# Optimization experiments

Hardware: AMD Instinct MI355X
Metric: run time of the kernel (lower is better)

## Reference

```python
import jax, jax.numpy as jnp
import numpy as np
import math

D = 768
H = 12
HD = D // H  # 64


def setup_inputs() -> dict:
    key = jax.random.key(0)
    ks = jax.random.split(key, 8)
    B, S = 32, 127
    desc = jax.random.normal(ks[0], (B, S, D), dtype=jnp.float32)
    nv = jax.random.normal(ks[1], (B, S + 1, D), dtype=jnp.float32)
    def xavier(k, shape):
        fan_in, fan_out = shape[1], shape[0]
        gain = 1.0 / math.sqrt(2.0)
        limit = gain * math.sqrt(6.0 / (fan_in + fan_out))
        return jax.random.uniform(k, shape, jnp.float32, -limit, limit)
    Wq = xavier(ks[2], (D, D)); bq = jnp.zeros((D,), jnp.float32)
    Wk = xavier(ks[3], (D, D)); bk = jnp.zeros((D,), jnp.float32)
    Wv = xavier(ks[4], (D, D)); bv = jnp.zeros((D,), jnp.float32)
    # attn_proj: Linear(3*head_dim, 1)
    Wa = xavier(ks[5], (1, 3 * HD))[0]  # [3*HD]
    ba = jnp.zeros((), jnp.float32)
    return {
        "desc_embeddings": desc,
        "name_value_embeddings": nv,
        "Wq": Wq, "bq": bq, "Wk": Wk, "bk": bk, "Wv": Wv, "bv": bv,
        "Wa": Wa, "ba": ba,
    }


def _forward(desc_embeddings, name_value_embeddings, Wq, bq, Wk, bk, Wv, bv, Wa, ba):
    B, new_seq, _ = name_value_embeddings.shape
    S = new_seq - 1

    # adjacency: var-var all ones, CLS->Var row = 1, Var->CLS col = 0, CLS->CLS = 0
    adj = jnp.zeros((new_seq, new_seq), jnp.float32)
    adj = adj.at[1:, 1:].set(1.0)
    adj = adj.at[0, 1:].set(1.0)
    adj = jnp.broadcast_to(adj, (B, new_seq, new_seq))

    # q,k,v: [B, H, new_seq, HD]
    def proj(W, b):
        y = name_value_embeddings @ W.T + b
        return y.reshape(B, new_seq, H, HD).transpose(0, 2, 1, 3)
    q = proj(Wq, bq); k = proj(Wk, bk); v = proj(Wv, bv)

    # attn_proj weight split: [q_part | k_part | edge_part], each [HD]
    wq_a, wk_a, we_a = Wa[:HD], Wa[HD:2 * HD], Wa[2 * HD:]

    # q/k scalar contributions per (b,h,i) and (b,h,j)
    lq = jnp.einsum('bhid,d->bhi', q, wq_a)  # [B,H,new_seq]
    lk = jnp.einsum('bhjd,d->bhj', k, wk_a)  # [B,H,new_seq]

    # edge_attr[b,i,j] per head h (head slice of concat[node_i_desc, node_j_desc]):
    # edge vector = concat(desc_i, desc_j)[h*HD:(h+1)*HD] viewed as [H, HD] of 2D dims.
    # concat(desc_i, desc_j) has 2D dims -> reshaped to [H, HD] means head h takes
    # slice [h*HD:(h+1)*HD] of the 2D-dim concat. Heads 0..H/2-1 come from desc_i,
    # heads H/2..H-1 come from desc_j. Compute edge dot with we_a accordingly.
    # desc_full[b,t] : [B,S,D]. Build per-head contributions:
    # for h < H//2: edge slice = desc_i[h*HD:(h+1)*HD]  -> depends only on i
    # for h >= H//2: edge slice = desc_j[(h-H//2)*HD:(h-H//2+1)*HD] -> depends only on j
    desc_heads = desc_embeddings.reshape(B, S, H // 2, 2 * HD)  # wrong split; do directly
    # Direct: per head h, slice indices into the 2D concat vector
    dh = desc_embeddings.reshape(B, S, H, HD)  # desc split into H chunks of HD (covers D = H*HD)
    # concat(desc_i,desc_j) reshaped to [H,HD]: heads 0..H/2-1 use dh_i[:, :, h],
    # heads H/2..H-1 use dh_j[:, :, h - H/2]
    e_dot = jnp.einsum('bshd,d->bsh', dh, jnp.broadcast_to(we_a, (HD,)))  # placeholder, recompute per head below
    # per-head edge scalar contribution for var-var edges:
    ei = jnp.einsum('bshd,d->bhs', dh, we_a)  # contribution if head slice comes from desc at position s
    Hh = H // 2
    # var-var logits edge part: for h<Hh depends on i; for h>=Hh depends on j
    le_i = ei[:, :Hh, :]   # [B,Hh,S] depends on i (row)
    le_j = ei[:, Hh:, :]   # [B,Hh,S] depends on j (col)

    # CLS edges: cls_edge_attr = concat(desc, desc) at position t (the var index)
    # row 0 (CLS->var j): edge = concat(desc_j, desc_j) -> head h slice:
    #   h<Hh: dh_j[h]; h>=Hh: dh_j[h-Hh]  -> scalar ei[b,h,j] with h mapped
    e_cls = jnp.concatenate([ei[:, :Hh, :], ei[:, :Hh, :]], axis=1) * 0  # init
    e_cls = jnp.concatenate([le_i, le_i], axis=1)  # [B,H,S]: head h<Hh uses dh[h], h>=Hh uses dh[h-Hh]
    # note ei[:, :Hh] corresponds to dh chunks 0..Hh-1 ; for h>=Hh slice is dh[h-Hh] -> same le_i

    # Assemble full logits [B,H,new_seq,new_seq]
    logits = lq[:, :, :, None] + lk[:, :, None, :]
    # edge contributions (only where adj==1; edge_attr zeroed elsewhere by mask mult)
    edge = jnp.zeros((B, H, new_seq, new_seq), jnp.float32)
    # var-var block [1:,1:]
    ev = jnp.zeros((B, H, S, S), jnp.float32)
    ev = ev + jnp.pad(le_i, ((0, 0), (0, Hh), (0, 0)))[:, :, :, None] * 0  # keep shapes
    ev_i = jnp.concatenate([le_i, jnp.zeros_like(le_j)], axis=1)  # h<Hh: i-dependent
    ev_j = jnp.concatenate([jnp.zeros_like(le_i), le_j], axis=1)  # h>=Hh: j-dependent
    ev = ev_i[:, :, :, None] + ev_j[:, :, None, :]  # [B,H,S,S]
    edge = edge.at[:, :, 1:, 1:].set(ev)
    # CLS row (0, 1:): cls_edge = concat(desc_j,desc_j); j = column var
    edge = edge.at[:, :, 0, 1:].set(e_cls)
    # CLS col (1:, 0): cls_edge = concat(desc_i,desc_i) BUT adj[:,1:,0]=0 so edge_attr
    # multiplied by adj -> zero; also masked out. edge stays 0, but torch zeroes it too.
    # mask edge by adjacency (edge_attr *= adj)
    edge = edge * adj[:, None, :, :]
    logits = logits + edge + ba

    mask = (adj[:, None, :, :] == 0).astype(jnp.float32) * -1e9
    logits = logits + mask
    attn = jax.nn.softmax(logits, axis=-1)  # [B,H,new_seq,new_seq]
    ctx = jnp.einsum('bhij,bhjd->bhid', attn, v)
    basis_outputs = ctx.transpose(0, 2, 1, 3)  # [B,new_seq,H,HD]
    return basis_outputs, attn


def reference(desc_embeddings, name_value_embeddings, Wq, bq, Wk, bk, Wv, bv, Wa, ba):
    return _forward(desc_embeddings, name_value_embeddings, Wq, bq, Wk, bk, Wv, bv, Wa, ba)
```

## Files before the change

### kernel.cpp

```cpp
#include <hip/hip_runtime.h>

#define NB 32
#define NS 128
#define SD 127
#define ND 768
#define NH 12
#define HD 64

__device__ inline float wredSum(float v){
  #pragma unroll
  for (int off=32; off>0; off>>=1) v += __shfl_xor(v, off);
  return v;
}
__device__ inline float wredMax(float v){
  #pragma unroll
  for (int off=32; off>0; off>>=1) v = fmaxf(v, __shfl_xor(v, off));
  return v;
}

__global__ __launch_bounds__(256)
void fold_ei(const float* __restrict__ Wk, const float* __restrict__ bk,
             const float* __restrict__ desc, const float* __restrict__ Wa,
             float* __restrict__ uk, float* __restrict__ bkdot,
             float* __restrict__ ei){
  int blk = blockIdx.x, t = threadIdx.x;
  int wave = t >> 6, lane = t & 63;
  if (blk < 144){
    __shared__ float red[4][64];
    int h = blk/12, cb = blk%12;
    int c0 = t & 63, dg = t >> 6;
    const float* base = Wk + (size_t)(h*HD + dg*16)*ND + cb*64 + c0;
    float acc = 0.f;
    #pragma unroll
    for (int i=0;i<16;++i) acc += base[(size_t)i*ND] * Wa[64 + dg*16 + i];
    red[dg][c0] = acc;
    __syncthreads();
    if (dg==0) uk[h*ND + cb*64 + c0] = red[0][c0]+red[1][c0]+red[2][c0]+red[3][c0];
    if (blk==0 && t < NH){
      float a = 0.f;
      for (int d=0; d<64; ++d) a += bk[t*HD+d]*Wa[64+d];
      bkdot[t] = a;
    }
  } else {
    int bs = blk - 144;
    int b = bs / SD, s = bs % SD;
    float wea = Wa[128 + lane];
    const float* row = desc + (size_t)bs * ND;
    #pragma unroll
    for (int hh=0; hh<3; ++hh){
      int h = wave + hh*4;
      float v = row[h*HD + lane] * wea;
      v = wredSum(v);
      if (lane==0) ei[(size_t)(b*NH + h)*NS + s] = v;
    }
  }
}

__global__ __launch_bounds__(256)
void lk_kernel(const float* __restrict__ nv, const float* __restrict__ uk,
               const float* __restrict__ bkdot, float* __restrict__ lk){
  __shared__ __align__(16) float S[4*ND];
  int blk = blockIdx.x, t = threadIdx.x, wave = t>>6, lane = t&63;
  float ukr[3][12], bkd[3];
  #pragma unroll
  for (int hh=0; hh<3; ++hh){
    int h = wave*3 + hh;
    bkd[hh] = bkdot[h];
    #pragma unroll
    for (int k=0;k<12;++k) ukr[hh][k] = uk[h*ND + lane + 64*k];
  }
  int j0 = blk*4;
  const float4* src = (const float4*)(nv + (size_t)j0*ND);
  ((float4*)S)[t]     = src[t];
  ((float4*)S)[t+256] = src[t+256];
  ((float4*)S)[t+512] = src[t+512];
  __syncthreads();
  float acc[12];
  #pragma unroll
  for (int rr=0; rr<4; ++rr)
    #pragma unroll
    for (int hh=0; hh<3; ++hh){
      float a = 0.f;
      #pragma unroll
      for (int k=0;k<12;++k) a += S[rr*ND + lane + 64*k]*ukr[hh][k];
      acc[rr*3+hh] = a;
    }
  #pragma unroll
  for (int i=0;i<12;++i) acc[i] = wredSum(acc[i]);
  if (lane == 0){
    int b = j0 >> 7, jb = j0 & 127;
    #pragma unroll
    for (int rr=0; rr<4; ++rr)
      #pragma unroll
      for (int hh=0; hh<3; ++hh)
        lk[(size_t)(b*NH + wave*3 + hh)*NS + jb + rr] = acc[rr*3+hh] + bkd[hh];
  }
}

__global__ __launch_bounds__(256)
void msoft_attn(const float* __restrict__ nv, const float* __restrict__ lk,
                const float* __restrict__ ei, float* __restrict__ m_part,
                float* __restrict__ out){
  int blk = blockIdx.x;
  int b = blk >> 4, jg = blk & 15;
  int t = threadIdx.x, wave = t >> 6, lane = t & 63;
  __shared__ float slk[NH*NS];
  __shared__ float sei[NH*NS];
  __shared__ float wf[24][NS];
  for (int i=t; i<NH*NS; i+=256) slk[i] = lk[(size_t)b*NH*NS + i];
  for (int i=t; i<NH*NS; i+=256) sei[i] = ei[(size_t)b*NH*NS + i];
  __syncthreads();
  #pragma unroll
  for (int rr=0; rr<6; ++rr){
    int r = wave*6 + rr;
    int h = r >> 1, which = r & 1;
    const float* eirow = (which==0) ? (sei + (h%6)*NS) : (sei + h*NS);
    float g = (which==0) ? 1.f : (h>=6 ? 1.f : 0.f);
    float x0 = (lane>=1) ? slk[h*NS+lane] + g*eirow[lane-1] : -3.0e38f;
    float x1 = slk[h*NS+lane+64] + g*eirow[lane+63];
    float mm = wredMax(fmaxf(x0,x1));
    float e0 = (lane>=1) ? __expf(x0-mm) : 0.f;
    float e1 = __expf(x1-mm);
    float s  = wredSum(e0+e1);
    float inv = 1.f/s;
    wf[r][lane]    = e0*inv;
    wf[r][lane+64] = e1*inv;
  }
  __syncthreads();
  if (t < 192){
    const float4* nvb = (const float4*)(nv + ((size_t)b*NS + jg*8)*ND);
    float4 acc[24];
    #pragma unroll
    for (int r=0;r<24;++r) acc[r] = make_float4(0.f,0.f,0.f,0.f);
    #pragma unroll
    for (int jj=0; jj<8; ++jj){
      float4 x = nvb[jj*192 + t];
      int j = jg*8 + jj;
      #pragma unroll
      for (int r=0;r<24;++r){
        float wr = wf[r][j];
        acc[r].x += wr*x.x; acc[r].y += wr*x.y;
        acc[r].z += wr*x.z; acc[r].w += wr*x.w;
      }
    }
    #pragma unroll
    for (int r=0;r<24;++r)
      ((float4*)(m_part + ((size_t)(b*24 + r)*16 + jg)*ND))[t] = acc[r];
  }
  float* abase = out + (size_t)NB*NS*ND + (size_t)(b*NH)*NS*NS;
  for (int idx=t; idx<3072; idx+=256){
    int h = idx >> 8;
    int rem = idx & 255;
    int il = rem >> 5, q = rem & 31;
    int i = jg*8 + il;
    const float* srcw = (i==0) ? wf[h*2] : wf[h*2+1];
    float4 v = { srcw[q*4], srcw[q*4+1], srcw[q*4+2], srcw[q*4+3] };
    ((float4*)(abase + (size_t)h*NS*NS))[i*32 + q] = v;
  }
}

__global__ __launch_bounds__(256)
void proj_basis(const float* __restrict__ m_part, const float* __restrict__ Wv,
                const float* __restrict__ bv, float* __restrict__ out){
  int bh = blockIdx.x;
  int b = bh / NH, h = bh % NH;
  int t = threadIdx.x, wave = t >> 6, lane = t & 63;
  __shared__ __align__(16) float msum[2*ND];
  __shared__ float cvec[2*HD];
  for (int i=t; i<384; i+=256){
    int rl = (i >= 192);
    int c4 = i - rl*192;
    const float4* mp = (const float4*)(m_part + ((size_t)(b*24 + h*2 + rl)*16)*ND) + c4;
    float4 s = make_float4(0.f,0.f,0.f,0.f);
    #pragma unroll
    for (int g=0; g<16; ++g){
      float4 v = mp[g*192];
      s.x += v.x; s.y += v.y; s.z += v.z; s.w += v.w;
    }
    ((float4*)msum)[i] = s;
  }
  __syncthreads();
  #pragma unroll
  for (int dd=0; dd<16; ++dd){
    int d = wave*16 + dd;
    const float* wvr = Wv + (size_t)(h*HD + d)*ND;
    float p0=0.f, p1=0.f;
    #pragma unroll
    for (int k=0; k<12; ++k){
      float wv = wvr[lane + 64*k];
      p0 += wv*msum[lane + 64*k];
      p1 += wv*msum[ND + lane + 64*k];
    }
    p0 = wredSum(p0); p1 = wredSum(p1);
    if (lane==0){
      float bb = bv[h*HD + d];
      cvec[d]    = p0 + bb;
      cvec[64+d] = p1 + bb;
    }
  }
  __syncthreads();
  float* bo = out + (size_t)b*NS*ND + h*HD;
  #pragma unroll
  for (int k=0;k<8;++k){
    int idx = t + k*256;
    int i = idx>>4, q = idx&15;
    const float* srcc = (i==0) ? cvec : cvec+64;
    float4 v = { srcc[q*4], srcc[q*4+1], srcc[q*4+2], srcc[q*4+3] };
    *(float4*)(bo + (size_t)i*ND + q*4) = v;
  }
}

extern "C" void kernel_launch(void* const* d_in, const int* in_sizes, int n_in,
                              void* d_out, int out_size, void* d_ws, size_t ws_size,
                              hipStream_t stream) {
  const float* desc = (const float*)d_in[0];
  const float* nv   = (const float*)d_in[1];
  const float* Wk   = (const float*)d_in[4];
  const float* bk   = (const float*)d_in[5];
  const float* Wv   = (const float*)d_in[6];
  const float* bv   = (const float*)d_in[7];
  const float* Wa   = (const float*)d_in[8];
  float* out = (float*)d_out;
  float* ws  = (float*)d_ws;

  float* uk     = ws;
  float* bkdot  = ws + 9216;
  float* eibuf  = ws + 9232;
  float* lkbuf  = ws + 58384;
  float* m_part = ws + 107536;

  fold_ei   <<<4208, 256, 0, stream>>>(Wk, bk, desc, Wa, uk, bkdot, eibuf);
  lk_kernel <<<1024, 256, 0, stream>>>(nv, uk, bkdot, lkbuf);
  msoft_attn<<<512,  256, 0, stream>>>(nv, lkbuf, eibuf, m_part, out);
  proj_basis<<<384,  256, 0, stream>>>(m_part, Wv, bv, out);
}
```

Before: 139.6 us.

## Store partial attention-weighted sums in bf16 and regroup ei with lk kernel

The partial weighted sums written by msoft_attn are now packed to bf16 and unpacked in proj_basis, halving that intermediate buffer's write and read traffic. The edge-scalar (ei) computation moves out of the Wk-folding kernel and into the lk kernel, so the tiny fold kernel runs alone and the desc-row reductions share a launch with lk. The bf16 rounding of partial sums adds precision loss to the basis outputs.

```diff
diff --git a/kernel.cpp b/kernel.cpp
--- a/kernel.cpp
+++ b/kernel.cpp
@@ -17,32 +17,80 @@
   for (int off=32; off>0; off>>=1) v = fmaxf(v, __shfl_xor(v, off));
   return v;
 }
-
-__global__ __launch_bounds__(256)
-void fold_ei(const float* __restrict__ Wk, const float* __restrict__ bk,
-             const float* __restrict__ desc, const float* __restrict__ Wa,
-             float* __restrict__ uk, float* __restrict__ bkdot,
-             float* __restrict__ ei){
+__device__ inline unsigned short f2bf(float x){
+  unsigned u = __float_as_uint(x);
+  u += 0x7fffu + ((u>>16)&1u);
+  return (unsigned short)(u>>16);
+}
+__device__ inline float bflo(unsigned v){ return __uint_as_float(v<<16); }
+__device__ inline float bfhi(unsigned v){ return __uint_as_float(v & 0xffff0000u); }
+
+__global__ __launch_bounds__(256)
+void fold_k(const float* __restrict__ Wk, const float* __restrict__ bk,
+            const float* __restrict__ Wa, float* __restrict__ uk,
+            float* __restrict__ bkdot){
   int blk = blockIdx.x, t = threadIdx.x;
-  int wave = t >> 6, lane = t & 63;
-  if (blk < 144){
-    __shared__ float red[4][64];
-    int h = blk/12, cb = blk%12;
-    int c0 = t & 63, dg = t >> 6;
-    const float* base = Wk + (size_t)(h*HD + dg*16)*ND + cb*64 + c0;
-    float acc = 0.f;
-    #pragma unroll
-    for (int i=0;i<16;++i) acc += base[(size_t)i*ND] * Wa[64 + dg*16 + i];
-    red[dg][c0] = acc;
+  __shared__ float red[4][64];
+  int h = blk/12, cb = blk%12;
+  int c0 = t & 63, dg = t >> 6;
+  const float* base = Wk + (size_t)(h*HD + dg*16)*ND + cb*64 + c0;
+  float acc = 0.f;
+  #pragma unroll
+  for (int i=0;i<16;++i) acc += base[(size_t)i*ND] * Wa[64 + dg*16 + i];
+  red[dg][c0] = acc;
+  __syncthreads();
+  if (dg==0) uk[h*ND + cb*64 + c0] = red[0][c0]+red[1][c0]+red[2][c0]+red[3][c0];
+  if (blk==0 && t < NH){
+    float a = 0.f;
+    for (int d=0; d<64; ++d) a += bk[t*HD+d]*Wa[64+d];
+    bkdot[t] = a;
+  }
+}
+
+__global__ __launch_bounds__(256)
+void lk_ei(const float* __restrict__ nv, const float* __restrict__ desc,
+           const float* __restrict__ uk, const float* __restrict__ bkdot,
+           const float* __restrict__ Wa,
+           float* __restrict__ lk, float* __restrict__ ei){
+  __shared__ __align__(16) float S[4*ND];
+  int blk = blockIdx.x, t = threadIdx.x, wave = t>>6, lane = t&63;
+  if (blk < 1024){
+    float ukr[3][12], bkd[3];
+    #pragma unroll
+    for (int hh=0; hh<3; ++hh){
+      int h = wave*3 + hh;
+      bkd[hh] = bkdot[h];
+      #pragma unroll
+      for (int k=0;k<12;++k) ukr[hh][k] = uk[h*ND + lane + 64*k];
+    }
+    int j0 = blk*4;
+    const float4* src = (const float4*)(nv + (size_t)j0*ND);
+    ((float4*)S)[t]     = src[t];
+    ((float4*)S)[t+256] = src[t+256];
+    ((float4*)S)[t+512] = src[t+512];
     __syncthreads();
-    if (dg==0) uk[h*ND + cb*64 + c0] = red[0][c0]+red[1][c0]+red[2][c0]+red[3][c0];
-    if (blk==0 && t < NH){
-      float a = 0.f;
-      for (int d=0; d<64; ++d) a += bk[t*HD+d]*Wa[64+d];
-      bkdot[t] = a;
+    float acc[12];
+    #pragma unroll
+    for (int rr=0; rr<4; ++rr)
+      #pragma unroll
+      for (int hh=0; hh<3; ++hh){
+        float a = 0.f;
+        #pragma unroll
+        for (int k=0;k<12;++k) a += S[rr*ND + lane + 64*k]*ukr[hh][k];
+        acc[rr*3+hh] = a;
+      }
+    #pragma unroll
+    for (int i=0;i<12;++i) acc[i] = wredSum(acc[i]);
+    if (lane == 0){
+      int b = j0 >> 7, jb = j0 & 127;
+      #pragma unroll
+      for (int rr=0; rr<4; ++rr)
+        #pragma unroll
+        for (int hh=0; hh<3; ++hh)
+          lk[(size_t)(b*NH + wave*3 + hh)*NS + jb + rr] = acc[rr*3+hh] + bkd[hh];
     }
   } else {
-    int bs = blk - 144;
+    int bs = blk - 1024;
     int b = bs / SD, s = bs % SD;
     float wea = Wa[128 + lane];
     const float* row = desc + (size_t)bs * ND;
@@ -57,49 +105,8 @@
 }
 
 __global__ __launch_bounds__(256)
-void lk_kernel(const float* __restrict__ nv, const float* __restrict__ uk,
-               const float* __restrict__ bkdot, float* __restrict__ lk){
-  __shared__ __align__(16) float S[4*ND];
-  int blk = blockIdx.x, t = threadIdx.x, wave = t>>6, lane = t&63;
-  float ukr[3][12], bkd[3];
-  #pragma unroll
-  for (int hh=0; hh<3; ++hh){
-    int h = wave*3 + hh;
-    bkd[hh] = bkdot[h];
-    #pragma unroll
-    for (int k=0;k<12;++k) ukr[hh][k] = uk[h*ND + lane + 64*k];
-  }
-  int j0 = blk*4;
-  const float4* src = (const float4*)(nv + (size_t)j0*ND);
-  ((float4*)S)[t]     = src[t];
-  ((float4*)S)[t+256] = src[t+256];
-  ((float4*)S)[t+512] = src[t+512];
-  __syncthreads();
-  float acc[12];
-  #pragma unroll
-  for (int rr=0; rr<4; ++rr)
-    #pragma unroll
-    for (int hh=0; hh<3; ++hh){
-      float a = 0.f;
-      #pragma unroll
-      for (int k=0;k<12;++k) a += S[rr*ND + lane + 64*k]*ukr[hh][k];
-      acc[rr*3+hh] = a;
-    }
-  #pragma unroll
-  for (int i=0;i<12;++i) acc[i] = wredSum(acc[i]);
-  if (lane == 0){
-    int b = j0 >> 7, jb = j0 & 127;
-    #pragma unroll
-    for (int rr=0; rr<4; ++rr)
-      #pragma unroll
-      for (int hh=0; hh<3; ++hh)
-        lk[(size_t)(b*NH + wave*3 + hh)*NS + jb + rr] = acc[rr*3+hh] + bkd[hh];
-  }
-}
-
-__global__ __launch_bounds__(256)
 void msoft_attn(const float* __restrict__ nv, const float* __restrict__ lk,
-                const float* __restrict__ ei, float* __restrict__ m_part,
+                const float* __restrict__ ei, unsigned short* __restrict__ m_part,
                 float* __restrict__ out){
   int blk = blockIdx.x;
   int b = blk >> 4, jg = blk & 15;
@@ -144,8 +151,10 @@
       }
     }
     #pragma unroll
-    for (int r=0;r<24;++r)
-      ((float4*)(m_part + ((size_t)(b*24 + r)*16 + jg)*ND))[t] = acc[r];
+    for (int r=0;r<24;++r){
+      ushort4 pk = { f2bf(acc[r].x), f2bf(acc[r].y), f2bf(acc[r].z), f2bf(acc[r].w) };
+      ((ushort4*)(m_part + ((size_t)(b*24 + r)*16 + jg)*ND))[t] = pk;
+    }
   }
   float* abase = out + (size_t)NB*NS*ND + (size_t)(b*NH)*NS*NS;
   for (int idx=t; idx<3072; idx+=256){
@@ -160,24 +169,26 @@
 }
 
 __global__ __launch_bounds__(256)
-void proj_basis(const float* __restrict__ m_part, const float* __restrict__ Wv,
-                const float* __restrict__ bv, float* __restrict__ out){
+void proj_basis(const unsigned short* __restrict__ m_part,
+                const float* __restrict__ Wv, const float* __restrict__ bv,
+                float* __restrict__ out){
   int bh = blockIdx.x;
   int b = bh / NH, h = bh % NH;
   int t = threadIdx.x, wave = t >> 6, lane = t & 63;
   __shared__ __align__(16) float msum[2*ND];
   __shared__ float cvec[2*HD];
-  for (int i=t; i<384; i+=256){
-    int rl = (i >= 192);
-    int c4 = i - rl*192;
-    const float4* mp = (const float4*)(m_part + ((size_t)(b*24 + h*2 + rl)*16)*ND) + c4;
-    float4 s = make_float4(0.f,0.f,0.f,0.f);
+  if (t < 192){
+    int rl = t / 96, c8 = t % 96;
+    const uint4* mp = (const uint4*)(m_part + ((size_t)(b*24 + h*2 + rl)*16)*ND) + c8;
+    float s[8] = {0.f,0.f,0.f,0.f,0.f,0.f,0.f,0.f};
     #pragma unroll
     for (int g=0; g<16; ++g){
-      float4 v = mp[g*192];
-      s.x += v.x; s.y += v.y; s.z += v.z; s.w += v.w;
-    }
-    ((float4*)msum)[i] = s;
+      uint4 v = mp[g*96];
+      s[0]+=bflo(v.x); s[1]+=bfhi(v.x); s[2]+=bflo(v.y); s[3]+=bfhi(v.y);
+      s[4]+=bflo(v.z); s[5]+=bfhi(v.z); s[6]+=bflo(v.w); s[7]+=bfhi(v.w);
+    }
+    #pragma unroll
+    for (int k=0;k<8;++k) msum[rl*ND + c8*8 + k] = s[k];
   }
   __syncthreads();
   #pragma unroll
@@ -227,10 +238,10 @@
   float* bkdot  = ws + 9216;
   float* eibuf  = ws + 9232;
   float* lkbuf  = ws + 58384;
-  float* m_part = ws + 107536;
-
-  fold_ei   <<<4208, 256, 0, stream>>>(Wk, bk, desc, Wa, uk, bkdot, eibuf);
-  lk_kernel <<<1024, 256, 0, stream>>>(nv, uk, bkdot, lkbuf);
+  unsigned short* m_part = (unsigned short*)(ws + 107536);
+
+  fold_k    <<<144,  256, 0, stream>>>(Wk, bk, Wa, uk, bkdot);
+  lk_ei     <<<5088, 256, 0, stream>>>(nv, desc, uk, bkdot, Wa, lkbuf, eibuf);
   msoft_attn<<<512,  256, 0, stream>>>(nv, lkbuf, eibuf, m_part, out);
   proj_basis<<<384,  256, 0, stream>>>(m_part, Wv, bv, out);
 }
```

Measured after the change: 141.6 us. About the same (+1.4%).
